# Kernel optimization log

Measured on AMD Instinct MI355X. Metric: run time of the kernel, lower is better.

Reference implementation:

```python
import jax, jax.numpy as jnp
from jax import lax
import numpy as np

B, C, H, W = 4, 64, 256, 256
OUT = 64


def setup_inputs() -> dict:
    key = jax.random.key(0)
    k1, k2, k3 = jax.random.split(key, 3)
    x = jax.random.normal(k1, (B, C, H, W), dtype=jnp.float32)
    # kaiming-ish init; offset conv scaled small so sampled offsets stay moderate
    w_off = jax.random.normal(k2, (18, C, 3, 3), dtype=jnp.float32) * 0.05
    b_off = jnp.zeros((18,), dtype=jnp.float32)
    w_def = jax.random.normal(k3, (OUT, C, 3, 3), dtype=jnp.float32) * (2.0 / (9 * C)) ** 0.5
    b_def = jnp.zeros((OUT,), dtype=jnp.float32)
    return {"x": x, "w_off": w_off, "b_off": b_off, "w_def": w_def, "b_def": b_def}


def _bilinear_sample(img, ys, xs):
    """img: [B,C,H,W]; ys,xs: [B,H,W] float sample coords. Zero padding outside."""
    y0 = jnp.floor(ys)
    x0 = jnp.floor(xs)
    ly = ys - y0  # [B,H,W]
    lx = xs - x0
    y0i = y0.astype(jnp.int32)
    x0i = x0.astype(jnp.int32)

    def corner(yi, xi):
        valid = (yi >= 0) & (yi < H) & (xi >= 0) & (xi < W)
        yc = jnp.clip(yi, 0, H - 1)
        xc = jnp.clip(xi, 0, W - 1)
        # gather per batch: [C,H,W] indexed by [H,W],[H,W] -> [C,H,W]
        v = jax.vmap(lambda im, a, b: im[:, a, b])(img, yc, xc)  # [B,C,H,W]
        return v * valid[:, None, :, :].astype(img.dtype)

    v00 = corner(y0i, x0i)
    v01 = corner(y0i, x0i + 1)
    v10 = corner(y0i + 1, x0i)
    v11 = corner(y0i + 1, x0i + 1)
    ly = ly[:, None, :, :]
    lx = lx[:, None, :, :]
    return (v00 * (1 - ly) * (1 - lx) + v01 * (1 - ly) * lx
            + v10 * ly * (1 - lx) + v11 * ly * lx)


def reference(x, w_off, b_off, w_def, b_def):
    # offset conv: 3x3, stride 1, pad 1 ('SAME')
    offsets = lax.conv_general_dilated(x, w_off, (1, 1), 'SAME') + b_off[None, :, None, None]
    offsets = offsets.reshape(B, 9, 2, H, W)  # per-tap (dy, dx), torchvision ordering

    hh = jnp.arange(H, dtype=x.dtype)[None, :, None]  # [1,H,1]
    ww = jnp.arange(W, dtype=x.dtype)[None, None, :]  # [1,1,W]

    out = jnp.zeros((B, OUT, H, W), dtype=x.dtype)
    for k in range(9):  # fixed small kernel loop
        ki, kj = k // 3, k % 3
        ys = hh + (ki - 1) + offsets[:, k, 0]  # pad=1 -> base = h + ki - 1
        xs = ww + (kj - 1) + offsets[:, k, 1]
        sampled = _bilinear_sample(x, ys, xs)  # [B,C,H,W]
        out = out + jnp.einsum('bchw,oc->bohw', sampled, w_def[:, :, ki, kj])
    return out + b_def[None, :, None, None]
```

## Files before the change

kernel.cpp:

```cpp
#include <hip/hip_runtime.h>


typedef _Float16 half8 __attribute__((ext_vector_type(8)));
typedef _Float16 h2    __attribute__((ext_vector_type(2)));
typedef float floatx4  __attribute__((ext_vector_type(4)));

namespace {
constexpr int B_ = 4, C_ = 64, H_ = 256, W_ = 256, OUT_ = 64;
constexpr int HW_ = H_ * W_;
constexpr size_t XT_BYTES = (size_t)B_ * HW_ * C_ * 2;
constexpr size_t WOFF_OFF = XT_BYTES;
constexpr int    WOFF_N   = 9 * 2 * 2 * 64 * 8;
constexpr size_t WDEF_OFF = WOFF_OFF + (size_t)WOFF_N * 2;
constexpr int    WDEF_N   = 9 * 2 * 4 * 64 * 8;
}

__global__ __launch_bounds__(256)
void transpose_x(const float* __restrict__ x, _Float16* __restrict__ xt,
                 const float* __restrict__ w_off, const float* __restrict__ w_def,
                 _Float16* __restrict__ wof, _Float16* __restrict__ wdf)
{
    const int bid = blockIdx.x;
    const int b = bid >> 8, y = bid & 255;
    const int px = threadIdx.x;
    const float* __restrict__ xp = x + (size_t)b * C_ * HW_ + y * W_ + px;

    union { _Float16 h[64]; uint4 u[8]; } v;
#pragma unroll
    for (int c = 0; c < C_; ++c) v.h[c] = (_Float16)xp[(size_t)c * HW_];

    _Float16* __restrict__ d0 = xt + ((size_t)(bid * 8) * 256 + px) * 8;
#pragma unroll
    for (int k = 0; k < 8; ++k)
        *(uint4*)(d0 + (size_t)k * 256 * 8) = v.u[k];

    if (bid < 32) {
        const int i0 = bid * 256 + threadIdx.x;
        for (int s = i0; s < OUT_ * C_ * 9; s += 8192) {
            const int n = s / 576;
            const int r = s - n * 576;
            const int c = r / 9;
            const int tap = r - c * 9;
            const int idx = ((((tap * 2 + (c >> 5)) * 4 + (n >> 4)) * 64
                              + ((c >> 3) & 3) * 16 + (n & 15)) << 3) + (c & 7);
            wdf[idx] = (_Float16)w_def[s];
        }
        for (int s = i0; s < 18 * C_ * 9; s += 8192) {
            const int n = s / 576;
            const int r = s - n * 576;
            const int c = r / 9;
            const int tap = r - c * 9;
            const int idx = ((((tap * 2 + (c >> 5)) * 2 + (n >> 4)) * 64
                              + ((c >> 3) & 3) * 16 + (n & 15)) << 3) + (c & 7);
            wof[idx] = (_Float16)w_off[s];
        }
        for (int i = i0; i < WOFF_N; i += 8192) {
            const int lane = (i >> 3) & 63, nt = (i >> 9) & 1;
            if (nt == 1 && (lane & 15) >= 2) wof[i] = (_Float16)0.0f;
        }
    }
}

__device__ __forceinline__ void bilin_setup(float ys, float xs, int* a, float* w)
{
    const float y0f = floorf(ys), x0f = floorf(xs);
    const float ly = ys - y0f, lx = xs - x0f;
    const int y0 = (int)y0f, x0 = (int)x0f;
    const int y1 = y0 + 1, x1 = x0 + 1;
    const int y0c = min(max(y0, 0), H_ - 1);
    const int y1c = min(max(y1, 0), H_ - 1);
    const int x0c = min(max(x0, 0), W_ - 1);
    const int x1c = min(max(x1, 0), W_ - 1);
    const float fy0 = (y0 >= 0 && y0 < H_) ? 1.0f : 0.0f;
    const float fy1 = (y1 >= 0 && y1 < H_) ? 1.0f : 0.0f;
    const float fx0 = (x0 >= 0 && x0 < W_) ? 1.0f : 0.0f;
    const float fx1 = (x1 >= 0 && x1 < W_) ? 1.0f : 0.0f;
    a[0] = y0c * 2048 + x0c;  w[0] = (1.0f - ly) * (1.0f - lx) * fy0 * fx0;
    a[1] = y0c * 2048 + x1c;  w[1] = (1.0f - ly) * lx          * fy0 * fx1;
    a[2] = y1c * 2048 + x0c;  w[2] = ly          * (1.0f - lx) * fy1 * fx0;
    a[3] = y1c * 2048 + x1c;  w[3] = ly          * lx          * fy1 * fx1;
}

__global__ __launch_bounds__(256, 4)
void deform_main(const _Float16* __restrict__ xt,
                 const _Float16* __restrict__ wof,
                 const float* __restrict__ b_off,
                 const _Float16* __restrict__ wdf,
                 const float* __restrict__ b_def,
                 float* __restrict__ out)
{
    __shared__ float off_lds[128 * 18];

    const int tid = threadIdx.x;
    const int lane = tid & 63;
    const int wv = tid >> 6;
    const int lm = lane & 15;
    const int lq = lane >> 4;
    const int bid = blockIdx.x;
    const int uid = (bid & 7) * 256 + (bid >> 3);
    const int colc = uid & 7;
    const int rowg = (uid >> 3) & 63;
    const int b = uid >> 9;
    const int y0 = rowg * 4;
    const int y = y0 + wv;
    const int base = colc * 32;
    const _Float16* __restrict__ xtb = xt + (size_t)b * HW_ * C_;

    {
        floatx4 acc1[2][2];
#pragma unroll
        for (int pt = 0; pt < 2; ++pt)
#pragma unroll
            for (int nt = 0; nt < 2; ++nt) acc1[pt][nt] = (floatx4)0.0f;

#pragma unroll
        for (int tap = 0; tap < 9; ++tap) {
            const int dy = tap / 3 - 1, dx = tap % 3 - 1;
            const int ys = y + dy;
            const bool yok = (unsigned)ys < 256u;
            const int ysc = min(max(ys, 0), 255);
#pragma unroll
            for (int kc = 0; kc < 2; ++kc) {
                half8 bfr[2];
#pragma unroll
                for (int nt = 0; nt < 2; ++nt)
                    bfr[nt] = *(const half8*)(wof +
                        ((size_t)(((tap * 2 + kc) * 2 + nt) * 64 + lane)) * 8);
                const int plane = (kc * 4 + lq) * 256;
#pragma unroll
                for (int pt = 0; pt < 2; ++pt) {
                    const int px_s = base + pt * 16 + lm + dx;
                    const bool vld = yok && ((unsigned)px_s < 256u);
                    const int pxc = min(max(px_s, 0), 255);
                    uint4 t = *(const uint4*)(xtb +
                        ((size_t)(ysc * 2048 + plane + pxc)) * 8);
                    if (!vld) { t.x = 0u; t.y = 0u; t.z = 0u; t.w = 0u; }
                    const half8 afr = __builtin_bit_cast(half8, t);
#pragma unroll
                    for (int nt = 0; nt < 2; ++nt)
                        acc1[pt][nt] = __builtin_amdgcn_mfma_f32_16x16x32_f16(
                            afr, bfr[nt], acc1[pt][nt], 0, 0, 0);
                }
            }
        }
#pragma unroll
        for (int nt = 0; nt < 2; ++nt) {
            const int j = nt * 16 + lm;
            if (j < 18) {
                const float bj = b_off[j];
#pragma unroll
                for (int pt = 0; pt < 2; ++pt) {
#pragma unroll
                    for (int r = 0; r < 4; ++r) {
                        const int lpx = wv * 32 + pt * 16 + lq * 4 + r;
                        off_lds[lpx * 18 + j] = acc1[pt][nt][r] + bj;
                    }
                }
            }
        }
    }
    __syncthreads();

    floatx4 acc[2][4];
#pragma unroll
    for (int pt = 0; pt < 2; ++pt)
#pragma unroll
        for (int ot = 0; ot < 4; ++ot) acc[pt][ot] = (floatx4)0.0f;

#pragma unroll
    for (int tap = 0; tap < 9; ++tap) {
        const int ki = tap / 3, kj = tap % 3;
        int ca[2][4];
        h2 cw[2][4];
#pragma unroll
        for (int pt = 0; pt < 2; ++pt) {
            const int lpx = wv * 32 + pt * 16 + lm;
            const float2 o2 = *(const float2*)&off_lds[lpx * 18 + tap * 2];
            const float ys = (float)(y + ki - 1) + o2.x;
            const float xs = (float)(base + pt * 16 + lm + kj - 1) + o2.y;
            float cwf[4];
            bilin_setup(ys, xs, ca[pt], cwf);
#pragma unroll
            for (int c = 0; c < 4; ++c) cw[pt][c] = (h2)((_Float16)cwf[c]);
        }

#pragma unroll
        for (int kc = 0; kc < 2; ++kc) {
            half8 bfr[4];
#pragma unroll
            for (int ot = 0; ot < 4; ++ot)
                bfr[ot] = *(const half8*)(wdf +
                    ((size_t)(((tap * 2 + kc) * 4 + ot) * 64 + lane)) * 8);

            const int plane = (kc * 4 + lq) * 256;
#pragma unroll
            for (int pt = 0; pt < 2; ++pt) {
                union Uc { uint4 u; h2 p[4]; } c0, c1, c2, c3;
                c0.u = *(const uint4*)(xtb + (size_t)(ca[pt][0] + plane) * 8);
                c1.u = *(const uint4*)(xtb + (size_t)(ca[pt][1] + plane) * 8);
                c2.u = *(const uint4*)(xtb + (size_t)(ca[pt][2] + plane) * 8);
                c3.u = *(const uint4*)(xtb + (size_t)(ca[pt][3] + plane) * 8);
                union Rr { h2 s[4]; half8 v; } r;
#pragma unroll
                for (int k = 0; k < 4; ++k)
                    r.s[k] = cw[pt][0] * c0.p[k] + cw[pt][1] * c1.p[k]
                           + cw[pt][2] * c2.p[k] + cw[pt][3] * c3.p[k];
#pragma unroll
                for (int ot = 0; ot < 4; ++ot)
                    acc[pt][ot] = __builtin_amdgcn_mfma_f32_16x16x32_f16(
                        r.v, bfr[ot], acc[pt][ot], 0, 0, 0);
            }
        }
    }

#pragma unroll
    for (int ot = 0; ot < 4; ++ot) {
        const int o = ot * 16 + lm;
        const float bd = b_def[o];
#pragma unroll
        for (int pt = 0; pt < 2; ++pt) {
            const int pxs = base + pt * 16 + lq * 4;
            const floatx4 a = acc[pt][ot];
            float4 v = make_float4(a[0] + bd, a[1] + bd, a[2] + bd, a[3] + bd);
            *(float4*)&out[(((size_t)b * OUT_ + o) * H_ + y) * W_ + pxs] = v;
        }
    }
}

extern "C" void kernel_launch(void* const* d_in, const int* in_sizes, int n_in,
                              void* d_out, int out_size, void* d_ws, size_t ws_size,
                              hipStream_t stream)
{
    const float* x     = (const float*)d_in[0];
    const float* w_off = (const float*)d_in[1];
    const float* b_off = (const float*)d_in[2];
    const float* w_def = (const float*)d_in[3];
    const float* b_def = (const float*)d_in[4];
    float* out = (float*)d_out;

    _Float16* xt  = (_Float16*)d_ws;
    _Float16* wof = (_Float16*)((char*)d_ws + WOFF_OFF);
    _Float16* wdf = (_Float16*)((char*)d_ws + WDEF_OFF);

    transpose_x<<<dim3(B_ * H_), dim3(256), 0, stream>>>(
        x, xt, w_off, w_def, wof, wdf);
    deform_main<<<dim3(B_ * H_ * 2), dim3(256), 0, stream>>>(
        xt, wof, b_off, wdf, b_def, out);
}
```

Baseline: 232.2 us.

## Halve per-wave pixel tile in deform kernel and vectorize transpose loads

The main deformable-conv kernel now gives each wave a single 16-pixel tile instead of two. It launches twice as many blocks and raises the occupancy hint from 4 to 5 waves per SIMD, using more parallelism to hide the latency of the scattered bilinear gathers. The transpose kernel now reads float4 vectors across 16 channels per thread instead of scalar per-channel loads. The trade-off is that each weight fragment is reused across fewer pixels, so weight loads per MFMA rise and scheduling overhead per block grows.

```diff
diff --git a/kernel.cpp b/kernel.cpp
--- a/kernel.cpp
+++ b/kernel.cpp
@@ -22,17 +22,28 @@
 {
     const int bid = blockIdx.x;
     const int b = bid >> 8, y = bid & 255;
-    const int px = threadIdx.x;
-    const float* __restrict__ xp = x + (size_t)b * C_ * HW_ + y * W_ + px;
-
-    union { _Float16 h[64]; uint4 u[8]; } v;
-#pragma unroll
-    for (int c = 0; c < C_; ++c) v.h[c] = (_Float16)xp[(size_t)c * HW_];
-
-    _Float16* __restrict__ d0 = xt + ((size_t)(bid * 8) * 256 + px) * 8;
-#pragma unroll
-    for (int k = 0; k < 8; ++k)
-        *(uint4*)(d0 + (size_t)k * 256 * 8) = v.u[k];
+    const int t64 = threadIdx.x & 63;
+    const int ch0 = (threadIdx.x >> 6) * 16;
+    const int pxg = t64 * 4;
+    const float* __restrict__ xp = x + (size_t)b * C_ * HW_ + y * W_ + pxg;
+
+#pragma unroll
+    for (int q = 0; q < 2; ++q) {
+        float4 f[8];
+#pragma unroll
+        for (int cc = 0; cc < 8; ++cc)
+            f[cc] = *(const float4*)&xp[(size_t)(ch0 + q * 8 + cc) * HW_];
+        const int kcq = (ch0 >> 3) + q;
+        _Float16* __restrict__ dg = xt + ((size_t)(bid * 8 + kcq) * 256 + pxg) * 8;
+#pragma unroll
+        for (int j = 0; j < 4; ++j) {
+            union { _Float16 h[8]; uint4 u; } g;
+#pragma unroll
+            for (int cc = 0; cc < 8; ++cc)
+                g.h[cc] = (_Float16)(((const float*)&f[cc])[j]);
+            *(uint4*)(dg + j * 8) = g.u;
+        }
+    }
 
     if (bid < 32) {
         const int i0 = bid * 256 + threadIdx.x;
@@ -81,7 +92,7 @@
     a[3] = y1c * 2048 + x1c;  w[3] = ly          * lx          * fy1 * fx1;
 }
 
-__global__ __launch_bounds__(256, 4)
+__global__ __launch_bounds__(256, 5)
 void deform_main(const _Float16* __restrict__ xt,
                  const _Float16* __restrict__ wof,
                  const float* __restrict__ b_off,
@@ -89,7 +100,7 @@
                  const float* __restrict__ b_def,
                  float* __restrict__ out)
 {
-    __shared__ float off_lds[128 * 18];
+    __shared__ float off_lds[64 * 18];
 
     const int tid = threadIdx.x;
     const int lane = tid & 63;
@@ -97,21 +108,17 @@
     const int lm = lane & 15;
     const int lq = lane >> 4;
     const int bid = blockIdx.x;
-    const int uid = (bid & 7) * 256 + (bid >> 3);
-    const int colc = uid & 7;
-    const int rowg = (uid >> 3) & 63;
-    const int b = uid >> 9;
-    const int y0 = rowg * 4;
-    const int y = y0 + wv;
-    const int base = colc * 32;
+    const int uid = (bid & 7) * 512 + (bid >> 3);
+    const int col = uid & 3;
+    const int y = (uid >> 2) & 255;
+    const int b = uid >> 10;
+    const int base = col * 64 + wv * 16;
     const _Float16* __restrict__ xtb = xt + (size_t)b * HW_ * C_;
 
     {
-        floatx4 acc1[2][2];
-#pragma unroll
-        for (int pt = 0; pt < 2; ++pt)
-#pragma unroll
-            for (int nt = 0; nt < 2; ++nt) acc1[pt][nt] = (floatx4)0.0f;
+        floatx4 acc1[2];
+#pragma unroll
+        for (int nt = 0; nt < 2; ++nt) acc1[nt] = (floatx4)0.0f;
 
 #pragma unroll
         for (int tap = 0; tap < 9; ++tap) {
@@ -127,20 +134,17 @@
                     bfr[nt] = *(const half8*)(wof +
                         ((size_t)(((tap * 2 + kc) * 2 + nt) * 64 + lane)) * 8);
                 const int plane = (kc * 4 + lq) * 256;
-#pragma unroll
-                for (int pt = 0; pt < 2; ++pt) {
-                    const int px_s = base + pt * 16 + lm + dx;
-                    const bool vld = yok && ((unsigned)px_s < 256u);
-                    const int pxc = min(max(px_s, 0), 255);
-                    uint4 t = *(const uint4*)(xtb +
-                        ((size_t)(ysc * 2048 + plane + pxc)) * 8);
-                    if (!vld) { t.x = 0u; t.y = 0u; t.z = 0u; t.w = 0u; }
-                    const half8 afr = __builtin_bit_cast(half8, t);
-#pragma unroll
-                    for (int nt = 0; nt < 2; ++nt)
-                        acc1[pt][nt] = __builtin_amdgcn_mfma_f32_16x16x32_f16(
-                            afr, bfr[nt], acc1[pt][nt], 0, 0, 0);
-                }
+                const int px_s = base + lm + dx;
+                const bool vld = yok && ((unsigned)px_s < 256u);
+                const int pxc = min(max(px_s, 0), 255);
+                uint4 t = *(const uint4*)(xtb +
+                    ((size_t)(ysc * 2048 + plane + pxc)) * 8);
+                if (!vld) { t.x = 0u; t.y = 0u; t.z = 0u; t.w = 0u; }
+                const half8 afr = __builtin_bit_cast(half8, t);
+#pragma unroll
+                for (int nt = 0; nt < 2; ++nt)
+                    acc1[nt] = __builtin_amdgcn_mfma_f32_16x16x32_f16(
+                        afr, bfr[nt], acc1[nt], 0, 0, 0);
             }
         }
 #pragma unroll
@@ -149,40 +153,32 @@
             if (j < 18) {
                 const float bj = b_off[j];
 #pragma unroll
-                for (int pt = 0; pt < 2; ++pt) {
-#pragma unroll
-                    for (int r = 0; r < 4; ++r) {
-                        const int lpx = wv * 32 + pt * 16 + lq * 4 + r;
-                        off_lds[lpx * 18 + j] = acc1[pt][nt][r] + bj;
-                    }
+                for (int r = 0; r < 4; ++r) {
+                    const int lpx = wv * 16 + lq * 4 + r;
+                    off_lds[lpx * 18 + j] = acc1[nt][r] + bj;
                 }
             }
         }
     }
     __syncthreads();
 
-    floatx4 acc[2][4];
-#pragma unroll
-    for (int pt = 0; pt < 2; ++pt)
-#pragma unroll
-        for (int ot = 0; ot < 4; ++ot) acc[pt][ot] = (floatx4)0.0f;
+    floatx4 acc[4];
+#pragma unroll
+    for (int ot = 0; ot < 4; ++ot) acc[ot] = (floatx4)0.0f;
 
 #pragma unroll
     for (int tap = 0; tap < 9; ++tap) {
         const int ki = tap / 3, kj = tap % 3;
-        int ca[2][4];
-        h2 cw[2][4];
-#pragma unroll
-        for (int pt = 0; pt < 2; ++pt) {
-            const int lpx = wv * 32 + pt * 16 + lm;
-            const float2 o2 = *(const float2*)&off_lds[lpx * 18 + tap * 2];
-            const float ys = (float)(y + ki - 1) + o2.x;
-            const float xs = (float)(base + pt * 16 + lm + kj - 1) + o2.y;
-            float cwf[4];
-            bilin_setup(ys, xs, ca[pt], cwf);
-#pragma unroll
-            for (int c = 0; c < 4; ++c) cw[pt][c] = (h2)((_Float16)cwf[c]);
-        }
+        const int lpx = wv * 16 + lm;
+        const float2 o2 = *(const float2*)&off_lds[lpx * 18 + tap * 2];
+        const float ys = (float)(y + ki - 1) + o2.x;
+        const float xs = (float)(col * 64 + lpx + kj - 1) + o2.y;
+        int ca[4];
+        float cwf[4];
+        bilin_setup(ys, xs, ca, cwf);
+        h2 cw[4];
+#pragma unroll
+        for (int c = 0; c < 4; ++c) cw[c] = (h2)((_Float16)cwf[c]);
 
 #pragma unroll
         for (int kc = 0; kc < 2; ++kc) {
@@ -193,23 +189,20 @@
                     ((size_t)(((tap * 2 + kc) * 4 + ot) * 64 + lane)) * 8);
 
             const int plane = (kc * 4 + lq) * 256;
-#pragma unroll
-            for (int pt = 0; pt < 2; ++pt) {
-                union Uc { uint4 u; h2 p[4]; } c0, c1, c2, c3;
-                c0.u = *(const uint4*)(xtb + (size_t)(ca[pt][0] + plane) * 8);
-                c1.u = *(const uint4*)(xtb + (size_t)(ca[pt][1] + plane) * 8);
-                c2.u = *(const uint4*)(xtb + (size_t)(ca[pt][2] + plane) * 8);
-                c3.u = *(const uint4*)(xtb + (size_t)(ca[pt][3] + plane) * 8);
-                union Rr { h2 s[4]; half8 v; } r;
-#pragma unroll
-                for (int k = 0; k < 4; ++k)
-                    r.s[k] = cw[pt][0] * c0.p[k] + cw[pt][1] * c1.p[k]
-                           + cw[pt][2] * c2.p[k] + cw[pt][3] * c3.p[k];
-#pragma unroll
-                for (int ot = 0; ot < 4; ++ot)
-                    acc[pt][ot] = __builtin_amdgcn_mfma_f32_16x16x32_f16(
-                        r.v, bfr[ot], acc[pt][ot], 0, 0, 0);
-            }
+            union Uc { uint4 u; h2 p[4]; } c0, c1, c2, c3;
+            c0.u = *(const uint4*)(xtb + (size_t)(ca[0] + plane) * 8);
+            c1.u = *(const uint4*)(xtb + (size_t)(ca[1] + plane) * 8);
+            c2.u = *(const uint4*)(xtb + (size_t)(ca[2] + plane) * 8);
+            c3.u = *(const uint4*)(xtb + (size_t)(ca[3] + plane) * 8);
+            union Rr { h2 s[4]; half8 v; } r;
+#pragma unroll
+            for (int k = 0; k < 4; ++k)
+                r.s[k] = cw[0] * c0.p[k] + cw[1] * c1.p[k]
+                       + cw[2] * c2.p[k] + cw[3] * c3.p[k];
+#pragma unroll
+            for (int ot = 0; ot < 4; ++ot)
+                acc[ot] = __builtin_amdgcn_mfma_f32_16x16x32_f16(
+                    r.v, bfr[ot], acc[ot], 0, 0, 0);
         }
     }
 
@@ -217,13 +210,10 @@
     for (int ot = 0; ot < 4; ++ot) {
         const int o = ot * 16 + lm;
         const float bd = b_def[o];
-#pragma unroll
-        for (int pt = 0; pt < 2; ++pt) {
-            const int pxs = base + pt * 16 + lq * 4;
-            const floatx4 a = acc[pt][ot];
-            float4 v = make_float4(a[0] + bd, a[1] + bd, a[2] + bd, a[3] + bd);
-            *(float4*)&out[(((size_t)b * OUT_ + o) * H_ + y) * W_ + pxs] = v;
-        }
+        const int pxs = base + lq * 4;
+        const floatx4 a = acc[ot];
+        float4 v = make_float4(a[0] + bd, a[1] + bd, a[2] + bd, a[3] + bd);
+        *(float4*)&out[(((size_t)b * OUT_ + o) * H_ + y) * W_ + pxs] = v;
     }
 }
 
@@ -244,6 +234,6 @@
 
     transpose_x<<<dim3(B_ * H_), dim3(256), 0, stream>>>(
         x, xt, w_off, w_def, wof, wdf);
-    deform_main<<<dim3(B_ * H_ * 2), dim3(256), 0, stream>>>(
+    deform_main<<<dim3(B_ * H_ * 4), dim3(256), 0, stream>>>(
         xt, wof, b_off, wdf, b_def, out);
 }
```

Measured after the change: 306.3 us. 1.32x slower.

## Software-pipeline gather loads in offset conv and deformable sampling loops

Applied to the files above, without the earlier changes.

Both phases of deform_main now use explicit double-buffered register prefetching. The global loads for the next (tap, channel-chunk) step are issued before the MFMAs of the current step, and the bilinear setup for the next tap is computed ahead of time. This is meant to hide gather latency behind compute within each wave. It raises register pressure, so the occupancy hint in launch_bounds drops from 4 to 3 waves, trading fewer resident waves for more in-flight loads per wave.

```diff
diff --git a/kernel.cpp b/kernel.cpp
--- a/kernel.cpp
+++ b/kernel.cpp
@@ -81,7 +81,7 @@
     a[3] = y1c * 2048 + x1c;  w[3] = ly          * lx          * fy1 * fx1;
 }
 
-__global__ __launch_bounds__(256, 4)
+__global__ __launch_bounds__(256, 3)
 void deform_main(const _Float16* __restrict__ xt,
                  const _Float16* __restrict__ wof,
                  const float* __restrict__ b_off,
@@ -113,36 +113,46 @@
 #pragma unroll
             for (int nt = 0; nt < 2; ++nt) acc1[pt][nt] = (floatx4)0.0f;
 
-#pragma unroll
-        for (int tap = 0; tap < 9; ++tap) {
-            const int dy = tap / 3 - 1, dx = tap % 3 - 1;
-            const int ys = y + dy;
-            const bool yok = (unsigned)ys < 256u;
-            const int ysc = min(max(ys, 0), 255);
-#pragma unroll
-            for (int kc = 0; kc < 2; ++kc) {
-                half8 bfr[2];
+        uint4 st1[2][2];
+        bool  v1[2][2];
+
+#define P1_ISSUE(TAP, KC, PAR) do {                                          \
+        const int dy_ = (TAP) / 3 - 1, dx_ = (TAP) % 3 - 1;                  \
+        const int ys_ = y + dy_;                                             \
+        const bool yok_ = (unsigned)ys_ < 256u;                              \
+        const int ysc_ = min(max(ys_, 0), 255);                              \
+        _Pragma("unroll")                                                    \
+        for (int pt_ = 0; pt_ < 2; ++pt_) {                                  \
+            const int pxs_ = base + pt_ * 16 + lm + dx_;                     \
+            v1[PAR][pt_] = yok_ && ((unsigned)pxs_ < 256u);                  \
+            const int pxc_ = min(max(pxs_, 0), 255);                         \
+            st1[PAR][pt_] = *(const uint4*)(xtb +                            \
+                (size_t)(ysc_ * 2048 + ((KC) * 4 + lq) * 256 + pxc_) * 8);   \
+        } } while (0)
+
+        P1_ISSUE(0, 0, 0);
+#pragma unroll
+        for (int g = 0; g < 18; ++g) {
+            const int tap = g >> 1, kc = g & 1, par = g & 1;
+            if (g < 17) { P1_ISSUE((g + 1) >> 1, (g + 1) & 1, (g + 1) & 1); }
+            half8 bfr[2];
+#pragma unroll
+            for (int nt = 0; nt < 2; ++nt)
+                bfr[nt] = *(const half8*)(wof +
+                    ((size_t)(((tap * 2 + kc) * 2 + nt) * 64 + lane)) * 8);
+#pragma unroll
+            for (int pt = 0; pt < 2; ++pt) {
+                uint4 t = st1[par][pt];
+                if (!v1[par][pt]) { t.x = 0u; t.y = 0u; t.z = 0u; t.w = 0u; }
+                const half8 afr = __builtin_bit_cast(half8, t);
 #pragma unroll
                 for (int nt = 0; nt < 2; ++nt)
-                    bfr[nt] = *(const half8*)(wof +
-                        ((size_t)(((tap * 2 + kc) * 2 + nt) * 64 + lane)) * 8);
-                const int plane = (kc * 4 + lq) * 256;
-#pragma unroll
-                for (int pt = 0; pt < 2; ++pt) {
-                    const int px_s = base + pt * 16 + lm + dx;
-                    const bool vld = yok && ((unsigned)px_s < 256u);
-                    const int pxc = min(max(px_s, 0), 255);
-                    uint4 t = *(const uint4*)(xtb +
-                        ((size_t)(ysc * 2048 + plane + pxc)) * 8);
-                    if (!vld) { t.x = 0u; t.y = 0u; t.z = 0u; t.w = 0u; }
-                    const half8 afr = __builtin_bit_cast(half8, t);
-#pragma unroll
-                    for (int nt = 0; nt < 2; ++nt)
-                        acc1[pt][nt] = __builtin_amdgcn_mfma_f32_16x16x32_f16(
-                            afr, bfr[nt], acc1[pt][nt], 0, 0, 0);
-                }
+                    acc1[pt][nt] = __builtin_amdgcn_mfma_f32_16x16x32_f16(
+                        afr, bfr[nt], acc1[pt][nt], 0, 0, 0);
             }
         }
+#undef P1_ISSUE
+
 #pragma unroll
         for (int nt = 0; nt < 2; ++nt) {
             const int j = nt * 16 + lm;
@@ -167,51 +177,76 @@
 #pragma unroll
         for (int ot = 0; ot < 4; ++ot) acc[pt][ot] = (floatx4)0.0f;
 
-#pragma unroll
-    for (int tap = 0; tap < 9; ++tap) {
-        const int ki = tap / 3, kj = tap % 3;
-        int ca[2][4];
-        h2 cw[2][4];
+    int   ca2[2][2][4];
+    h2    cw2[2][2][4];
+    uint4 stc[2][2][4];
+
+#define P2_BILIN(TAP, TP) do {                                               \
+        const int ki_ = (TAP) / 3, kj_ = (TAP) % 3;                          \
+        _Pragma("unroll")                                                    \
+        for (int pt_ = 0; pt_ < 2; ++pt_) {                                  \
+            const int lpx_ = wv * 32 + pt_ * 16 + lm;                        \
+            const float2 o2_ = *(const float2*)&off_lds[lpx_ * 18 + (TAP) * 2]; \
+            const float ys_ = (float)(y + ki_ - 1) + o2_.x;                  \
+            const float xs_ = (float)(base + pt_ * 16 + lm + kj_ - 1) + o2_.y; \
+            float cwf_[4];                                                   \
+            bilin_setup(ys_, xs_, ca2[TP][pt_], cwf_);                       \
+            _Pragma("unroll")                                                \
+            for (int c_ = 0; c_ < 4; ++c_)                                   \
+                cw2[TP][pt_][c_] = (h2)((_Float16)cwf_[c_]);                 \
+        } } while (0)
+
+#define P2_ISSUE(TP, KC, PAR) do {                                           \
+        const int plane_ = ((KC) * 4 + lq) * 256;                            \
+        _Pragma("unroll")                                                    \
+        for (int pt_ = 0; pt_ < 2; ++pt_)                                    \
+            _Pragma("unroll")                                                \
+            for (int c_ = 0; c_ < 4; ++c_)                                   \
+                stc[PAR][pt_][c_] = *(const uint4*)(xtb +                    \
+                    (size_t)(ca2[TP][pt_][c_] + plane_) * 8);                \
+        } while (0)
+
+    P2_BILIN(0, 0);
+    P2_ISSUE(0, 0, 0);
+
+#pragma unroll
+    for (int g = 0; g < 18; ++g) {
+        const int tap = g >> 1, kc = g & 1, par = g & 1, tp = (g >> 1) & 1;
+
+        if (kc == 0) {
+            P2_ISSUE(tp, 1, 1);
+        } else if (tap < 8) {
+            P2_ISSUE(tp ^ 1, 0, 0);
+        }
+
+        half8 bfr[4];
+#pragma unroll
+        for (int ot = 0; ot < 4; ++ot)
+            bfr[ot] = *(const half8*)(wdf +
+                ((size_t)(((tap * 2 + kc) * 4 + ot) * 64 + lane)) * 8);
+
+        if (kc == 0 && tap < 8) P2_BILIN(tap + 1, tp ^ 1);
+
 #pragma unroll
         for (int pt = 0; pt < 2; ++pt) {
-            const int lpx = wv * 32 + pt * 16 + lm;
-            const float2 o2 = *(const float2*)&off_lds[lpx * 18 + tap * 2];
-            const float ys = (float)(y + ki - 1) + o2.x;
-            const float xs = (float)(base + pt * 16 + lm + kj - 1) + o2.y;
-            float cwf[4];
-            bilin_setup(ys, xs, ca[pt], cwf);
-#pragma unroll
-            for (int c = 0; c < 4; ++c) cw[pt][c] = (h2)((_Float16)cwf[c]);
-        }
-
-#pragma unroll
-        for (int kc = 0; kc < 2; ++kc) {
-            half8 bfr[4];
+            union Uc { uint4 u; h2 p[4]; } cc0, cc1, cc2, cc3;
+            cc0.u = stc[par][pt][0];
+            cc1.u = stc[par][pt][1];
+            cc2.u = stc[par][pt][2];
+            cc3.u = stc[par][pt][3];
+            union Rr { h2 s[4]; half8 v; } r;
+#pragma unroll
+            for (int k = 0; k < 4; ++k)
+                r.s[k] = cw2[tp][pt][0] * cc0.p[k] + cw2[tp][pt][1] * cc1.p[k]
+                       + cw2[tp][pt][2] * cc2.p[k] + cw2[tp][pt][3] * cc3.p[k];
 #pragma unroll
             for (int ot = 0; ot < 4; ++ot)
-                bfr[ot] = *(const half8*)(wdf +
-                    ((size_t)(((tap * 2 + kc) * 4 + ot) * 64 + lane)) * 8);
-
-            const int plane = (kc * 4 + lq) * 256;
-#pragma unroll
-            for (int pt = 0; pt < 2; ++pt) {
-                union Uc { uint4 u; h2 p[4]; } c0, c1, c2, c3;
-                c0.u = *(const uint4*)(xtb + (size_t)(ca[pt][0] + plane) * 8);
-                c1.u = *(const uint4*)(xtb + (size_t)(ca[pt][1] + plane) * 8);
-                c2.u = *(const uint4*)(xtb + (size_t)(ca[pt][2] + plane) * 8);
-                c3.u = *(const uint4*)(xtb + (size_t)(ca[pt][3] + plane) * 8);
-                union Rr { h2 s[4]; half8 v; } r;
-#pragma unroll
-                for (int k = 0; k < 4; ++k)
-                    r.s[k] = cw[pt][0] * c0.p[k] + cw[pt][1] * c1.p[k]
-                           + cw[pt][2] * c2.p[k] + cw[pt][3] * c3.p[k];
-#pragma unroll
-                for (int ot = 0; ot < 4; ++ot)
-                    acc[pt][ot] = __builtin_amdgcn_mfma_f32_16x16x32_f16(
-                        r.v, bfr[ot], acc[pt][ot], 0, 0, 0);
-            }
-        }
-    }
+                acc[pt][ot] = __builtin_amdgcn_mfma_f32_16x16x32_f16(
+                    r.v, bfr[ot], acc[pt][ot], 0, 0, 0);
+        }
+    }
+#undef P2_BILIN
+#undef P2_ISSUE
 
 #pragma unroll
     for (int ot = 0; ot < 4; ++ot) {
```

New measurement: 224.8 us. 1.03x faster.
